# Kernel tuning notes

Hardware: AMD Instinct MI355X
Metric: run time of the kernel (lower is better)

The kernel has to match this reference:

```python
import jax, jax.numpy as jnp
import numpy as np

B = 8192
I_SIZE = 1024
H_SIZE = 1024
C2 = 2.7183  # module's hard-coded e approximation

def setup_inputs() -> dict:
    key = jax.random.key(0)
    k0, k1, k2, k3, k4 = jax.random.split(key, 5)
    input_tensor = jax.random.uniform(k0, (B, I_SIZE + 1), dtype=jnp.float32)  # last col = dt >= 0
    h_cur = jax.random.normal(k1, (B, H_SIZE), dtype=jnp.float32)
    c_cur = jax.random.normal(k2, (B, H_SIZE), dtype=jnp.float32)
    W_layers = jax.random.normal(k3, (4 * H_SIZE, I_SIZE + H_SIZE), dtype=jnp.float32) * 0.02
    b_layers = jnp.zeros((4 * H_SIZE,), dtype=jnp.float32)
    W_desc = jax.random.normal(k4, (H_SIZE, H_SIZE), dtype=jnp.float32) * 0.02
    b_desc = jnp.zeros((H_SIZE,), dtype=jnp.float32)
    return {"input_tensor": input_tensor, "h_cur": h_cur, "c_cur": c_cur,
            "W_layers": W_layers, "b_layers": b_layers,
            "W_desc": W_desc, "b_desc": b_desc}

def reference(input_tensor, h_cur, c_cur, W_layers, b_layers, W_desc, b_desc):
    x = input_tensor[:, :-1]          # [B, I]
    dt = input_tensor[:, -1:]         # [B, 1]
    # map_elapse_time: T = 1/log(t + e), broadcast over h_size (matmul with ones == broadcast)
    T = 1.0 / jnp.log(dt + C2)        # [B, 1]
    C_ST = jnp.tanh(h_cur @ W_desc.T + b_desc)          # [B, H]
    h_adj = h_cur - C_ST + T * C_ST                     # decayed short-term memory
    combined = jnp.concatenate([x, h_adj], axis=1)      # [B, I+H]
    gates = combined @ W_layers.T + b_layers            # [B, 4H]
    cc_i, cc_f, cc_o, cc_g = jnp.split(gates, 4, axis=1)
    i = jax.nn.sigmoid(cc_i)
    f = jax.nn.sigmoid(cc_f)
    o = jax.nn.sigmoid(cc_o)
    g = jnp.tanh(cc_g)
    c_next = f * c_cur + i * g
    h_next = o * jnp.tanh(c_next)
    return (h_next, c_next)
```

## Files before the change

kernel.cpp:

```cpp
#include <hip/hip_runtime.h>
#include <hip/hip_bf16.h>
#include <math.h>

typedef __bf16 bf16x8 __attribute__((ext_vector_type(8)));
typedef float  f32x4  __attribute__((ext_vector_type(4)));

#define B_ROWS 8192
#define HSZ    1024

#define GLOAD16(gsrc, ldst)                                                          \
  __builtin_amdgcn_global_load_lds((const __attribute__((address_space(1))) void*)(gsrc), \
                                   (__attribute__((address_space(3))) void*)(ldst),  \
                                   16, 0, 0)

__device__ inline unsigned short f2bf(float f) {
  union { float f; unsigned u; } x; x.f = f;
  unsigned r = x.u + 0x7fffu + ((x.u >> 16) & 1u);
  return (unsigned short)(r >> 16);
}

__device__ inline void store4bf(unsigned short* p, float4 v) {
  ushort4 u;
  u.x = f2bf(v.x); u.y = f2bf(v.y); u.z = f2bf(v.z); u.w = f2bf(v.w);
  *(ushort4*)p = u;
}

__device__ inline float sigm(float x) { return 1.0f / (1.0f + __expf(-x)); }

__global__ void k_convert(const float* __restrict__ inp,
                          const float* __restrict__ h,
                          const float* __restrict__ Wl,
                          const float* __restrict__ Wd,
                          unsigned short* __restrict__ comb,
                          unsigned short* __restrict__ Wlb,
                          unsigned short* __restrict__ hb,
                          unsigned short* __restrict__ Wdb,
                          float* __restrict__ Tm1) {
  const long stride = (long)gridDim.x * blockDim.x;
  const long tid0 = (long)blockIdx.x * blockDim.x + threadIdx.x;

  for (long i = tid0; i < (long)B_ROWS * HSZ / 4; i += stride) {
    float4 v = ((const float4*)h)[i];
    store4bf(hb + i * 4, v);
  }
  for (long i = tid0; i < (long)B_ROWS * HSZ / 4; i += stride) {
    long e = i * 4; long b = e >> 10; long c = e & 1023;
    float4 v = *(const float4*)(inp + b * 1025 + c);
    store4bf(comb + b * 2048 + c, v);
  }
  for (long i = tid0; i < 4096L * 2048 / 4; i += stride) {
    float4 v = ((const float4*)Wl)[i];
    store4bf(Wlb + i * 4, v);
  }
  for (long i = tid0; i < 1024L * 1024 / 4; i += stride) {
    float4 v = ((const float4*)Wd)[i];
    store4bf(Wdb + i * 4, v);
  }
  for (long i = tid0; i < B_ROWS; i += stride) {
    float dt = inp[i * 1025 + 1024];
    Tm1[i] = 1.0f / logf(dt + 2.7183f) - 1.0f;
  }
}

__global__ void k_gemm1(const unsigned short* __restrict__ A,
                        const unsigned short* __restrict__ Bm,
                        const float* __restrict__ h,
                        const float* __restrict__ bd,
                        const float* __restrict__ Tm1,
                        unsigned short* __restrict__ comb) {
  const int K = 1024;
  __shared__ __align__(16) unsigned short As[128 * 32];
  __shared__ __align__(16) unsigned short Bs[128 * 32];
  const int tid = threadIdx.x;
  const int lane = tid & 63;
  const int wave = tid >> 6;
  const int wr = wave >> 1, wc = wave & 1;
  const int bRow = blockIdx.x;
  const int bCol = blockIdx.y;

  const int sRow = tid >> 2;
  const int sK = (tid & 3) * 8;
  const unsigned short* aSrc0 = A + (long)(bRow * 128 + sRow) * K + sK;
  const unsigned short* aSrc1 = A + (long)(bRow * 128 + 64 + sRow) * K + sK;
  const unsigned short* bSrc0 = Bm + (long)(bCol * 128 + sRow) * K + sK;
  const unsigned short* bSrc1 = Bm + (long)(bCol * 128 + 64 + sRow) * K + sK;
  unsigned short* aDst0 = As + tid * 8;
  unsigned short* aDst1 = As + 2048 + tid * 8;
  unsigned short* bDst0 = Bs + tid * 8;
  unsigned short* bDst1 = Bs + 2048 + tid * 8;

  f32x4 acc[4][4] = {};
  const int fr = lane & 15, fk = (lane >> 4) * 8;

  for (int k0 = 0; k0 < K; k0 += 32) {
    GLOAD16(aSrc0 + k0, aDst0);
    GLOAD16(aSrc1 + k0, aDst1);
    GLOAD16(bSrc0 + k0, bDst0);
    GLOAD16(bSrc1 + k0, bDst1);
    __syncthreads();
    bf16x8 a[4], b[4];
#pragma unroll
    for (int m = 0; m < 4; m++) a[m] = *(const bf16x8*)(As + (wr * 64 + m * 16 + fr) * 32 + fk);
#pragma unroll
    for (int n = 0; n < 4; n++) b[n] = *(const bf16x8*)(Bs + (wc * 64 + n * 16 + fr) * 32 + fk);
#pragma unroll
    for (int m = 0; m < 4; m++)
#pragma unroll
      for (int n = 0; n < 4; n++)
        acc[m][n] = __builtin_amdgcn_mfma_f32_16x16x32_bf16(a[m], b[n], acc[m][n], 0, 0, 0);
    __syncthreads();
  }

  const int cr = (lane >> 4) * 4;
  const int cc = lane & 15;
#pragma unroll
  for (int m = 0; m < 4; m++)
#pragma unroll
    for (int n = 0; n < 4; n++) {
      const int col = bCol * 128 + wc * 64 + n * 16 + cc;
#pragma unroll
      for (int r = 0; r < 4; r++) {
        const int row = bRow * 128 + wr * 64 + m * 16 + cr + r;
        float v = acc[m][n][r] + bd[col];
        float cst = tanhf(v);
        float hadj = h[(long)row * HSZ + col] + Tm1[row] * cst;
        comb[(long)row * 2048 + 1024 + col] = f2bf(hadj);
      }
    }
}

__global__ void k_gemm2(const unsigned short* __restrict__ A,
                        const unsigned short* __restrict__ Bm,
                        const float* __restrict__ bl,
                        const float* __restrict__ c_cur,
                        float* __restrict__ out) {
  const int K = 2048;
  __shared__ __align__(16) unsigned short As[128 * 32];
  __shared__ __align__(16) unsigned short Bs[128 * 32];
  const int tid = threadIdx.x;
  const int lane = tid & 63;
  const int wave = tid >> 6;
  const int wr = wave >> 1, wc = wave & 1;
  const int bRow = blockIdx.x;
  const int bj = blockIdx.y;

  const int sRow = tid >> 2;
  const int sK = (tid & 3) * 8;
  const int rl0 = sRow, rl1 = 64 + sRow;
  const unsigned short* aSrc0 = A + (long)(bRow * 128 + sRow) * K + sK;
  const unsigned short* aSrc1 = A + (long)(bRow * 128 + 64 + sRow) * K + sK;
  const unsigned short* bSrc0 = Bm + (long)((rl0 >> 5) * 1024 + bj * 32 + (rl0 & 31)) * K + sK;
  const unsigned short* bSrc1 = Bm + (long)((rl1 >> 5) * 1024 + bj * 32 + (rl1 & 31)) * K + sK;
  unsigned short* aDst0 = As + tid * 8;
  unsigned short* aDst1 = As + 2048 + tid * 8;
  unsigned short* bDst0 = Bs + tid * 8;
  unsigned short* bDst1 = Bs + 2048 + tid * 8;

  f32x4 acc[4][4] = {};
  const int fr = lane & 15, fk = (lane >> 4) * 8;

  for (int k0 = 0; k0 < K; k0 += 32) {
    GLOAD16(aSrc0 + k0, aDst0);
    GLOAD16(aSrc1 + k0, aDst1);
    GLOAD16(bSrc0 + k0, bDst0);
    GLOAD16(bSrc1 + k0, bDst1);
    __syncthreads();
    bf16x8 a[4], b[4];
#pragma unroll
    for (int m = 0; m < 4; m++) a[m] = *(const bf16x8*)(As + (wr * 64 + m * 16 + fr) * 32 + fk);
#pragma unroll
    for (int n = 0; n < 4; n++) b[n] = *(const bf16x8*)(Bs + (n * 32 + wc * 16 + fr) * 32 + fk);
#pragma unroll
    for (int m = 0; m < 4; m++)
#pragma unroll
      for (int n = 0; n < 4; n++)
        acc[m][n] = __builtin_amdgcn_mfma_f32_16x16x32_bf16(a[m], b[n], acc[m][n], 0, 0, 0);
    __syncthreads();
  }

  const int cr = (lane >> 4) * 4;
  const int cc = lane & 15;
  const int j = bj * 32 + wc * 16 + cc;
#pragma unroll
  for (int m = 0; m < 4; m++) {
#pragma unroll
    for (int r = 0; r < 4; r++) {
      const int row = bRow * 128 + wr * 64 + m * 16 + cr + r;
      float iv = sigm(acc[m][0][r] + bl[j]);
      float fv = sigm(acc[m][1][r] + bl[1024 + j]);
      float ov = sigm(acc[m][2][r] + bl[2048 + j]);
      float gv = tanhf(acc[m][3][r] + bl[3072 + j]);
      float cn = fv * c_cur[(long)row * HSZ + j] + iv * gv;
      float hn = ov * tanhf(cn);
      out[(long)row * HSZ + j] = hn;
      out[(long)B_ROWS * HSZ + (long)row * HSZ + j] = cn;
    }
  }
}

extern "C" void kernel_launch(void* const* d_in, const int* in_sizes, int n_in,
                              void* d_out, int out_size, void* d_ws, size_t ws_size,
                              hipStream_t stream) {
  const float* inp = (const float*)d_in[0];
  const float* h   = (const float*)d_in[1];
  const float* c   = (const float*)d_in[2];
  const float* Wl  = (const float*)d_in[3];
  const float* bl  = (const float*)d_in[4];
  const float* Wd  = (const float*)d_in[5];
  const float* bd  = (const float*)d_in[6];

  char* ws = (char*)d_ws;
  unsigned short* comb = (unsigned short*)(ws);
  unsigned short* Wlb  = (unsigned short*)(ws + 33554432);
  unsigned short* hb   = (unsigned short*)(ws + 50331648);
  unsigned short* Wdb  = (unsigned short*)(ws + 67108864);
  float*          Tm1  = (float*)(ws + 69206016);
  float*          out  = (float*)d_out;

  hipLaunchKernelGGL(k_convert, dim3(2048), dim3(256), 0, stream,
                     inp, h, Wl, Wd, comb, Wlb, hb, Wdb, Tm1);
  hipLaunchKernelGGL(k_gemm1, dim3(64, 8), dim3(256), 0, stream,
                     hb, Wdb, h, bd, Tm1, comb);
  hipLaunchKernelGGL(k_gemm2, dim3(64, 32), dim3(256), 0, stream,
                     comb, Wlb, bl, c, out);
}
```

Measured before the change: 259.4 us.

## Triple-buffer GEMM K-loop with swizzled LDS and XCD-aware block mapping

```diff
diff --git a/kernel.cpp b/kernel.cpp
--- a/kernel.cpp
+++ b/kernel.cpp
@@ -17,12 +17,6 @@
   union { float f; unsigned u; } x; x.f = f;
   unsigned r = x.u + 0x7fffu + ((x.u >> 16) & 1u);
   return (unsigned short)(r >> 16);
-}
-
-__device__ inline void store4bf(unsigned short* p, float4 v) {
-  ushort4 u;
-  u.x = f2bf(v.x); u.y = f2bf(v.y); u.z = f2bf(v.z); u.w = f2bf(v.w);
-  *(ushort4*)p = u;
 }
 
 __device__ inline float sigm(float x) { return 1.0f / (1.0f + __expf(-x)); }
@@ -39,77 +33,117 @@
   const long stride = (long)gridDim.x * blockDim.x;
   const long tid0 = (long)blockIdx.x * blockDim.x + threadIdx.x;
 
-  for (long i = tid0; i < (long)B_ROWS * HSZ / 4; i += stride) {
-    float4 v = ((const float4*)h)[i];
-    store4bf(hb + i * 4, v);
-  }
-  for (long i = tid0; i < (long)B_ROWS * HSZ / 4; i += stride) {
-    long e = i * 4; long b = e >> 10; long c = e & 1023;
-    float4 v = *(const float4*)(inp + b * 1025 + c);
-    store4bf(comb + b * 2048 + c, v);
-  }
-  for (long i = tid0; i < 4096L * 2048 / 4; i += stride) {
-    float4 v = ((const float4*)Wl)[i];
-    store4bf(Wlb + i * 4, v);
-  }
-  for (long i = tid0; i < 1024L * 1024 / 4; i += stride) {
-    float4 v = ((const float4*)Wd)[i];
-    store4bf(Wdb + i * 4, v);
+#define CNV8(dst, s0, s1) { ushort4 u0, u1;                                   \
+    u0.x = f2bf(s0.x); u0.y = f2bf(s0.y); u0.z = f2bf(s0.z); u0.w = f2bf(s0.w); \
+    u1.x = f2bf(s1.x); u1.y = f2bf(s1.y); u1.z = f2bf(s1.z); u1.w = f2bf(s1.w); \
+    *(ushort4*)(dst) = u0; *(ushort4*)((dst) + 4) = u1; }
+
+  for (long i = tid0; i < (long)B_ROWS * HSZ / 8; i += stride) {
+    float4 v0 = ((const float4*)h)[i * 2], v1 = ((const float4*)h)[i * 2 + 1];
+    CNV8(hb + i * 8, v0, v1);
+  }
+  for (long i = tid0; i < (long)B_ROWS * HSZ / 8; i += stride) {
+    long e = i * 8; long b = e >> 10; long c = e & 1023;
+    const float* s = inp + b * 1025 + c;
+    float4 v0 = *(const float4*)s, v1 = *(const float4*)(s + 4);
+    CNV8(comb + b * 2048 + c, v0, v1);
+  }
+  for (long i = tid0; i < 4096L * 2048 / 8; i += stride) {
+    float4 v0 = ((const float4*)Wl)[i * 2], v1 = ((const float4*)Wl)[i * 2 + 1];
+    CNV8(Wlb + i * 8, v0, v1);
+  }
+  for (long i = tid0; i < 1024L * 1024 / 8; i += stride) {
+    float4 v0 = ((const float4*)Wd)[i * 2], v1 = ((const float4*)Wd)[i * 2 + 1];
+    CNV8(Wdb + i * 8, v0, v1);
   }
   for (long i = tid0; i < B_ROWS; i += stride) {
     float dt = inp[i * 1025 + 1024];
     Tm1[i] = 1.0f / logf(dt + 2.7183f) - 1.0f;
   }
-}
-
-__global__ void k_gemm1(const unsigned short* __restrict__ A,
-                        const unsigned short* __restrict__ Bm,
-                        const float* __restrict__ h,
-                        const float* __restrict__ bd,
-                        const float* __restrict__ Tm1,
-                        unsigned short* __restrict__ comb) {
-  const int K = 1024;
-  __shared__ __align__(16) unsigned short As[128 * 32];
-  __shared__ __align__(16) unsigned short Bs[128 * 32];
+#undef CNV8
+}
+
+
+#define NT1 32
+__global__ __launch_bounds__(256, 3)
+void k_gemm1_fr(const unsigned short* __restrict__ A,
+                const unsigned short* __restrict__ Bm,
+                const float* __restrict__ h,
+                const float* __restrict__ bd,
+                const float* __restrict__ Tm1,
+                unsigned short* __restrict__ comb) {
+  __shared__ __align__(16) unsigned short lds[3][8192];
+
   const int tid = threadIdx.x;
   const int lane = tid & 63;
-  const int wave = tid >> 6;
-  const int wr = wave >> 1, wc = wave & 1;
-  const int bRow = blockIdx.x;
-  const int bCol = blockIdx.y;
-
-  const int sRow = tid >> 2;
-  const int sK = (tid & 3) * 8;
-  const unsigned short* aSrc0 = A + (long)(bRow * 128 + sRow) * K + sK;
-  const unsigned short* aSrc1 = A + (long)(bRow * 128 + 64 + sRow) * K + sK;
-  const unsigned short* bSrc0 = Bm + (long)(bCol * 128 + sRow) * K + sK;
-  const unsigned short* bSrc1 = Bm + (long)(bCol * 128 + 64 + sRow) * K + sK;
-  unsigned short* aDst0 = As + tid * 8;
-  unsigned short* aDst1 = As + 2048 + tid * 8;
-  unsigned short* bDst0 = Bs + tid * 8;
-  unsigned short* bDst1 = Bs + 2048 + tid * 8;
+  const int wid = tid >> 6;
+  const int wr = wid >> 1, wc = wid & 1;
+
+  const int bid = blockIdx.x;
+  const int xcd = bid & 7;
+  const int ii = bid >> 3;
+  const int bRow = xcd * 8 + (ii & 7);
+  const int bCol = ii >> 3;
+
+  const int sr = tid >> 2;
+  const int swsel = (sr >> 1) & 3;
+  const int gk = ((tid & 3) ^ swsel) << 3;
+  const unsigned short* aS0 = A + (long)(bRow * 128 + sr) * 1024 + gk;
+  const unsigned short* aS1 = A + (long)(bRow * 128 + 64 + sr) * 1024 + gk;
+  const unsigned short* bS0 = Bm + (long)(bCol * 128 + sr) * 1024 + gk;
+  const unsigned short* bS1 = Bm + (long)(bCol * 128 + 64 + sr) * 1024 + gk;
+
+#define STG1(slot, tt) {                                                  \
+    GLOAD16(aS0 + (long)(tt) * 32, &lds[slot][0    + tid * 8]);           \
+    GLOAD16(aS1 + (long)(tt) * 32, &lds[slot][2048 + tid * 8]);           \
+    GLOAD16(bS0 + (long)(tt) * 32, &lds[slot][4096 + tid * 8]);           \
+    GLOAD16(bS1 + (long)(tt) * 32, &lds[slot][6144 + tid * 8]); }
+
+  const int fr = lane & 15, q = lane >> 4;
+  int offA[4], offB[4];
+#pragma unroll
+  for (int m = 0; m < 4; m++) {
+    const int row = wr * 64 + m * 16 + fr;
+    offA[m] = row * 32 + ((q ^ ((row >> 1) & 3)) << 3);
+  }
+#pragma unroll
+  for (int n = 0; n < 4; n++) {
+    const int row = wc * 64 + n * 16 + fr;
+    offB[n] = 4096 + row * 32 + ((q ^ ((row >> 1) & 3)) << 3);
+  }
 
   f32x4 acc[4][4] = {};
-  const int fr = lane & 15, fk = (lane >> 4) * 8;
-
-  for (int k0 = 0; k0 < K; k0 += 32) {
-    GLOAD16(aSrc0 + k0, aDst0);
-    GLOAD16(aSrc1 + k0, aDst1);
-    GLOAD16(bSrc0 + k0, bDst0);
-    GLOAD16(bSrc1 + k0, bDst1);
-    __syncthreads();
-    bf16x8 a[4], b[4];
-#pragma unroll
-    for (int m = 0; m < 4; m++) a[m] = *(const bf16x8*)(As + (wr * 64 + m * 16 + fr) * 32 + fk);
-#pragma unroll
-    for (int n = 0; n < 4; n++) b[n] = *(const bf16x8*)(Bs + (wc * 64 + n * 16 + fr) * 32 + fk);
-#pragma unroll
-    for (int m = 0; m < 4; m++)
-#pragma unroll
-      for (int n = 0; n < 4; n++)
-        acc[m][n] = __builtin_amdgcn_mfma_f32_16x16x32_bf16(a[m], b[n], acc[m][n], 0, 0, 0);
-    __syncthreads();
-  }
+
+  STG1(0, 0); STG1(1, 1);
+
+#define BODY1(t, SLOT, VM)                                                          \
+  {                                                                                 \
+    asm volatile("s_waitcnt vmcnt(" #VM ")" ::: "memory");                          \
+    __builtin_amdgcn_s_barrier();                                                   \
+    if ((t) + 2 < NT1) STG1(((t) + 2) % 3, (t) + 2);                                \
+    const unsigned short* buf = &lds[SLOT][0];                                      \
+    bf16x8 aF[4], bF[4];                                                            \
+    _Pragma("unroll")                                                               \
+    for (int n = 0; n < 4; n++) bF[n] = *(const bf16x8*)(buf + offB[n]);            \
+    _Pragma("unroll")                                                               \
+    for (int m = 0; m < 4; m++) aF[m] = *(const bf16x8*)(buf + offA[m]);            \
+    __builtin_amdgcn_s_setprio(1);                                                  \
+    _Pragma("unroll")                                                               \
+    for (int m = 0; m < 4; m++)                                                     \
+      _Pragma("unroll")                                                             \
+      for (int n = 0; n < 4; n++)                                                   \
+        acc[m][n] = __builtin_amdgcn_mfma_f32_16x16x32_bf16(aF[m], bF[n], acc[m][n], 0, 0, 0); \
+    __builtin_amdgcn_s_setprio(0);                                                  \
+  }
+
+  for (int t = 0; t < 30; t += 3) {
+    BODY1(t,     0, 4);
+    BODY1(t + 1, 1, 4);
+    BODY1(t + 2, 2, 4);
+  }
+  BODY1(30, 0, 4);
+  BODY1(31, 1, 0);
+#undef BODY1
 
   const int cr = (lane >> 4) * 4;
   const int cc = lane & 15;
@@ -129,58 +163,89 @@
     }
 }
 
-__global__ void k_gemm2(const unsigned short* __restrict__ A,
-                        const unsigned short* __restrict__ Bm,
-                        const float* __restrict__ bl,
-                        const float* __restrict__ c_cur,
-                        float* __restrict__ out) {
-  const int K = 2048;
-  __shared__ __align__(16) unsigned short As[128 * 32];
-  __shared__ __align__(16) unsigned short Bs[128 * 32];
+#define NT2 64
+__global__ __launch_bounds__(256, 3)
+void k_gemm2_fr(const unsigned short* __restrict__ A,
+                const unsigned short* __restrict__ Bm,
+                const float* __restrict__ bl,
+                const float* __restrict__ c_cur,
+                float* __restrict__ out) {
+  __shared__ __align__(16) unsigned short lds[3][8192];
+
   const int tid = threadIdx.x;
   const int lane = tid & 63;
-  const int wave = tid >> 6;
-  const int wr = wave >> 1, wc = wave & 1;
-  const int bRow = blockIdx.x;
-  const int bj = blockIdx.y;
-
-  const int sRow = tid >> 2;
-  const int sK = (tid & 3) * 8;
-  const int rl0 = sRow, rl1 = 64 + sRow;
-  const unsigned short* aSrc0 = A + (long)(bRow * 128 + sRow) * K + sK;
-  const unsigned short* aSrc1 = A + (long)(bRow * 128 + 64 + sRow) * K + sK;
-  const unsigned short* bSrc0 = Bm + (long)((rl0 >> 5) * 1024 + bj * 32 + (rl0 & 31)) * K + sK;
-  const unsigned short* bSrc1 = Bm + (long)((rl1 >> 5) * 1024 + bj * 32 + (rl1 & 31)) * K + sK;
-  unsigned short* aDst0 = As + tid * 8;
-  unsigned short* aDst1 = As + 2048 + tid * 8;
-  unsigned short* bDst0 = Bs + tid * 8;
-  unsigned short* bDst1 = Bs + 2048 + tid * 8;
+  const int wid = tid >> 6;
+  const int wr = wid >> 1, wc = wid & 1;
+
+  const int bid = blockIdx.x;
+  const int xcd = bid & 7;
+  const int ii = bid >> 3;
+  const int bCol = xcd * 4 + (ii & 3);
+  const int bRow = ii >> 2;
+
+  const int sr = tid >> 2;
+  const int swsel = (sr >> 1) & 3;
+  const int gk = ((tid & 3) ^ swsel) << 3;
+  const unsigned short* aS0 = A + (long)(bRow * 128 + sr) * 2048 + gk;
+  const unsigned short* aS1 = A + (long)(bRow * 128 + 64 + sr) * 2048 + gk;
+  const int grow0 = ((sr >> 4) & 3) * 1024 + bCol * 32 + (sr & 15);
+  const unsigned short* bS0 = Bm + (long)grow0 * 2048 + gk;
+  const unsigned short* bS1 = Bm + (long)(grow0 + 16) * 2048 + gk;
+
+#define STG2(slot, tt) {                                                  \
+    GLOAD16(aS0 + (long)(tt) * 32, &lds[slot][0    + tid * 8]);           \
+    GLOAD16(aS1 + (long)(tt) * 32, &lds[slot][2048 + tid * 8]);           \
+    GLOAD16(bS0 + (long)(tt) * 32, &lds[slot][4096 + tid * 8]);           \
+    GLOAD16(bS1 + (long)(tt) * 32, &lds[slot][6144 + tid * 8]); }
+
+  const int fr = lane & 15, q = lane >> 4;
+  int offA[4], offB[4];
+#pragma unroll
+  for (int m = 0; m < 4; m++) {
+    const int row = wr * 64 + m * 16 + fr;
+    offA[m] = row * 32 + ((q ^ ((row >> 1) & 3)) << 3);
+  }
+#pragma unroll
+  for (int n = 0; n < 4; n++) {
+    const int row = wc * 64 + n * 16 + fr;
+    offB[n] = 4096 + row * 32 + ((q ^ ((row >> 1) & 3)) << 3);
+  }
 
   f32x4 acc[4][4] = {};
-  const int fr = lane & 15, fk = (lane >> 4) * 8;
-
-  for (int k0 = 0; k0 < K; k0 += 32) {
-    GLOAD16(aSrc0 + k0, aDst0);
-    GLOAD16(aSrc1 + k0, aDst1);
-    GLOAD16(bSrc0 + k0, bDst0);
-    GLOAD16(bSrc1 + k0, bDst1);
-    __syncthreads();
-    bf16x8 a[4], b[4];
-#pragma unroll
-    for (int m = 0; m < 4; m++) a[m] = *(const bf16x8*)(As + (wr * 64 + m * 16 + fr) * 32 + fk);
-#pragma unroll
-    for (int n = 0; n < 4; n++) b[n] = *(const bf16x8*)(Bs + (n * 32 + wc * 16 + fr) * 32 + fk);
-#pragma unroll
-    for (int m = 0; m < 4; m++)
-#pragma unroll
-      for (int n = 0; n < 4; n++)
-        acc[m][n] = __builtin_amdgcn_mfma_f32_16x16x32_bf16(a[m], b[n], acc[m][n], 0, 0, 0);
-    __syncthreads();
-  }
+
+  STG2(0, 0); STG2(1, 1);
+
+#define BODY2(t, SLOT, VM)                                                          \
+  {                                                                                 \
+    asm volatile("s_waitcnt vmcnt(" #VM ")" ::: "memory");                          \
+    __builtin_amdgcn_s_barrier();                                                   \
+    if ((t) + 2 < NT2) STG2(((t) + 2) % 3, (t) + 2);                                \
+    const unsigned short* buf = &lds[SLOT][0];                                      \
+    bf16x8 aF[4], bF[4];                                                            \
+    _Pragma("unroll")                                                               \
+    for (int n = 0; n < 4; n++) bF[n] = *(const bf16x8*)(buf + offB[n]);            \
+    _Pragma("unroll")                                                               \
+    for (int m = 0; m < 4; m++) aF[m] = *(const bf16x8*)(buf + offA[m]);            \
+    __builtin_amdgcn_s_setprio(1);                                                  \
+    _Pragma("unroll")                                                               \
+    for (int m = 0; m < 4; m++)                                                     \
+      _Pragma("unroll")                                                             \
+      for (int n = 0; n < 4; n++)                                                   \
+        acc[m][n] = __builtin_amdgcn_mfma_f32_16x16x32_bf16(aF[m], bF[n], acc[m][n], 0, 0, 0); \
+    __builtin_amdgcn_s_setprio(0);                                                  \
+  }
+
+  for (int t = 0; t < 63; t += 3) {
+    BODY2(t,     0, 4);
+    BODY2(t + 1, 1, 4);
+    BODY2(t + 2, 2, 4);
+  }
+  BODY2(63, 0, 0);
+#undef BODY2
 
   const int cr = (lane >> 4) * 4;
   const int cc = lane & 15;
-  const int j = bj * 32 + wc * 16 + cc;
+  const int j = bCol * 32 + wc * 16 + cc;
 #pragma unroll
   for (int m = 0; m < 4; m++) {
 #pragma unroll
@@ -219,8 +284,8 @@
 
   hipLaunchKernelGGL(k_convert, dim3(2048), dim3(256), 0, stream,
                      inp, h, Wl, Wd, comb, Wlb, hb, Wdb, Tm1);
-  hipLaunchKernelGGL(k_gemm1, dim3(64, 8), dim3(256), 0, stream,
+  hipLaunchKernelGGL(k_gemm1_fr, dim3(512), dim3(256), 0, stream,
                      hb, Wdb, h, bd, Tm1, comb);
-  hipLaunchKernelGGL(k_gemm2, dim3(64, 32), dim3(256), 0, stream,
+  hipLaunchKernelGGL(k_gemm2_fr, dim3(2048), dim3(256), 0, stream,
                      comb, Wlb, bl, c, out);
 }
```

Measured after the change: 240.4 us. -7.3%, faster.
